# Kernel tuning notes

Hardware: AMD Instinct MI355X
Metric: run time of the kernel (lower is better)

Reference implementation:

```python
import jax, jax.numpy as jnp
import numpy as np

N = 1_000_000   # total nodes
H = 128         # hidden_dim
B = 16_384      # num graphs in batch


def setup_inputs() -> dict:
    key = jax.random.key(0)
    k0, k1, k2, k3 = jax.random.split(key, 4)
    x = jax.random.normal(k0, (N, H), dtype=jnp.float32)
    batch_index = jnp.sort(jax.random.randint(k1, (N,), 0, B))
    s = 1.0 / np.sqrt(H)
    W1 = jax.random.normal(k2, (H, H), dtype=jnp.float32) * s
    b1 = jnp.zeros((H,), dtype=jnp.float32)
    W2 = jax.random.normal(k3, (H, 1), dtype=jnp.float32) * s
    b2 = jnp.zeros((1,), dtype=jnp.float32)
    return {"x": x, "W1": W1, "b1": b1, "W2": W2, "b2": b2,
            "batch_index": batch_index, "num_graphs": B}


def reference(x, W1, b1, W2, b2, batch_index, num_graphs):
    # --- global mean pool ---
    seg_sum = jax.ops.segment_sum(x, batch_index, num_segments=num_graphs)
    counts = jax.ops.segment_sum(jnp.ones((x.shape[0],), x.dtype), batch_index,
                                 num_segments=num_graphs)
    mean = seg_sum / jnp.maximum(counts, 1.0)[:, None]          # [B, H]
    # --- global max pool ---
    mx = jax.ops.segment_max(x, batch_index, num_segments=num_graphs)  # [B, H]
    # --- attentional aggregation: gate MLP -> segment softmax -> weighted sum ---
    h = jax.nn.silu(x @ W1 + b1)                                # [N, H]
    gate = (h @ W2 + b2)[:, 0]                                  # [N]
    gmax = jax.ops.segment_max(gate, batch_index, num_segments=num_graphs)
    e = jnp.exp(gate - gmax[batch_index])
    denom = jax.ops.segment_sum(e, batch_index, num_segments=num_graphs)
    att = e / denom[batch_index]                                # [N] per-segment softmax
    attn_out = jax.ops.segment_sum(att[:, None] * x, batch_index,
                                   num_segments=num_graphs)     # [B, H]
    return jnp.concatenate([mean, mx, attn_out], axis=-1)       # [B, 3H]
```

## Files before the change

### kernel.cpp

```cpp
#include <hip/hip_runtime.h>
#include <hip/hip_bf16.h>
#include <math.h>

#define H 128
#define TILE 64
#define XB_STRIDE 136

typedef __attribute__((ext_vector_type(8))) short bf16x8;
typedef __attribute__((ext_vector_type(4))) float f32x4;

__device__ __forceinline__ short f2bf(float f) {
  union { float f; unsigned u; } v; v.f = f;
  unsigned r = v.u + 0x7fffu + ((v.u >> 16) & 1u);
  return (short)(r >> 16);
}

__global__ void prep_kernel(const float* __restrict__ w1, short* __restrict__ w1t) {
  int i = blockIdx.x * blockDim.x + threadIdx.x;
  if (i >= H * H) return;
  int k = i >> 7, n = i & (H - 1);
  w1t[n * H + k] = f2bf(w1[k * H + n]);
}

__global__ void bounds_kernel(const int* __restrict__ bi, int* __restrict__ seg_start,
                              int N, int B) {
  int n = blockIdx.x * blockDim.x + threadIdx.x;
  if (n >= N) return;
  int cur = bi[n];
  int prev = (n == 0) ? -1 : bi[n - 1];
  for (int g = prev + 1; g <= cur; ++g) seg_start[g] = n;
  if (n == N - 1) {
    for (int g = cur + 1; g <= B; ++g) seg_start[g] = N;
  }
}

__global__ __launch_bounds__(256) void fused_kernel(
    const float* __restrict__ x, const short* __restrict__ w1t,
    const float* __restrict__ b1, const float* __restrict__ w2,
    const float* __restrict__ b2, const int* __restrict__ seg_start,
    float* __restrict__ out)
{
  __shared__ __align__(16) float xf[TILE][H];
  __shared__ __align__(16) short xb[TILE * XB_STRIDE];
  __shared__ float gate_lds[TILE];
  __shared__ float merge_lds[5][H];

  const int g = blockIdx.x;
  const int s = seg_start[g];
  const int e = seg_start[g + 1];
  const int R = e - s;

  const int tid  = threadIdx.x;
  const int w    = tid >> 6;
  const int lane = tid & 63;
  const int l15  = lane & 15;
  const int q    = lane >> 4;

  const int h    = tid & (H - 1);
  const int half = tid >> 7;
  float sum = 0.f, mx = -INFINITY;
  float m_run = -INFINITY, l_run = 0.f, accv = 0.f;

  const float b2v  = b2[0];
  const int   c0   = 32 * w + l15, c1 = c0 + 16;
  const float w2c0 = w2[c0], w2c1 = w2[c1];
  const float b1c0 = b1[c0], b1c1 = b1[c1];

  for (int t0 = 0; t0 < R; t0 += TILE) {
    const int Rt = min(TILE, R - t0);

    {
      const int colg = (tid & 31) * 4;
      const int row0 = tid >> 5;
#pragma unroll
      for (int i = 0; i < 8; ++i) {
        int row = row0 + 8 * i;
        float4 v = make_float4(0.f, 0.f, 0.f, 0.f);
        if (row < Rt) v = *(const float4*)(x + (size_t)(s + t0 + row) * H + colg);
        *(float4*)(&xf[row][colg]) = v;
        short4 sv = make_short4(f2bf(v.x), f2bf(v.y), f2bf(v.z), f2bf(v.w));
        *(short4*)(&xb[row * XB_STRIDE + colg]) = sv;
      }
    }
    if (tid < TILE) gate_lds[tid] = 0.0f;
    __syncthreads();

    f32x4 acc[4][2] = {};
#pragma unroll
    for (int kc = 0; kc < H; kc += 32) {
      bf16x8 a[4], b[2];
#pragma unroll
      for (int mt = 0; mt < 4; ++mt)
        a[mt] = *(const bf16x8*)(&xb[(16 * mt + l15) * XB_STRIDE + kc + 8 * q]);
#pragma unroll
      for (int nt = 0; nt < 2; ++nt) {
        int n = 32 * w + 16 * nt + l15;
        b[nt] = *(const bf16x8*)(w1t + n * H + kc + 8 * q);
      }
#pragma unroll
      for (int mt = 0; mt < 4; ++mt)
#pragma unroll
        for (int nt = 0; nt < 2; ++nt)
          acc[mt][nt] = __builtin_amdgcn_mfma_f32_16x16x32_bf16(a[mt], b[nt], acc[mt][nt], 0, 0, 0);
    }

#pragma unroll
    for (int mt = 0; mt < 4; ++mt) {
#pragma unroll
      for (int r = 0; r < 4; ++r) {
        float h0 = acc[mt][0][r] + b1c0;
        float h1 = acc[mt][1][r] + b1c1;
        float s0 = h0 / (1.0f + __expf(-h0));
        float s1 = h1 / (1.0f + __expf(-h1));
        float p = s0 * w2c0 + s1 * w2c1;
        p += __shfl_xor(p, 1);
        p += __shfl_xor(p, 2);
        p += __shfl_xor(p, 4);
        p += __shfl_xor(p, 8);
        if (l15 == 0) atomicAdd(&gate_lds[16 * mt + 4 * q + r], p);
      }
    }
    __syncthreads();

    for (int r = half; r < Rt; r += 2) {
      float gt = gate_lds[r] + b2v;
      float xv = xf[r][h];
      sum += xv;
      mx = fmaxf(mx, xv);
      float m_new = fmaxf(m_run, gt);
      float corr = __expf(m_run - m_new);
      float ev   = __expf(gt - m_new);
      l_run = l_run * corr + ev;
      accv  = accv * corr + ev * xv;
      m_run = m_new;
    }
    __syncthreads();
  }

  if (half == 1) {
    merge_lds[0][h] = sum;
    merge_lds[1][h] = mx;
    merge_lds[2][h] = m_run;
    merge_lds[3][h] = l_run;
    merge_lds[4][h] = accv;
  }
  __syncthreads();
  if (half == 0) {
    float sum2 = merge_lds[0][h], mx2 = merge_lds[1][h];
    float m2 = merge_lds[2][h], l2 = merge_lds[3][h], a2 = merge_lds[4][h];
    sum += sum2;
    mx = fmaxf(mx, mx2);
    float m_new = fmaxf(m_run, m2);
    float cA = __expf(m_run - m_new);
    float cB = __expf(m2 - m_new);
    l_run = l_run * cA + l2 * cB;
    accv  = accv * cA + a2 * cB;

    float* og = out + (size_t)g * (3 * H);
    og[h]         = sum / fmaxf((float)R, 1.0f);
    og[H + h]     = mx;
    og[2 * H + h] = (R > 0) ? (accv / l_run) : 0.0f;
  }
}

extern "C" void kernel_launch(void* const* d_in, const int* in_sizes, int n_in,
                              void* d_out, int out_size, void* d_ws, size_t ws_size,
                              hipStream_t stream)
{
  const float* x   = (const float*)d_in[0];
  const float* w1  = (const float*)d_in[1];
  const float* b1  = (const float*)d_in[2];
  const float* w2  = (const float*)d_in[3];
  const float* b2  = (const float*)d_in[4];
  const int*  bidx = (const int*)d_in[5];

  const int N  = in_sizes[5];
  const int Bn = out_size / (3 * H);

  char* ws = (char*)d_ws;
  size_t off = 0;
  int* seg_start = (int*)(ws + off);
  off += (size_t)(Bn + 1) * sizeof(int);
  off = (off + 255) & ~(size_t)255;
  short* w1t = (short*)(ws + off);

  prep_kernel<<<(H * H + 255) / 256, 256, 0, stream>>>(w1, w1t);
  bounds_kernel<<<(N + 255) / 256, 256, 0, stream>>>(bidx, seg_start, N, Bn);
  fused_kernel<<<Bn, 256, 0, stream>>>(x, w1t, b1, w2, b2, seg_start, (float*)d_out);
}
```

Before: 884.0 us.

## Keep x tile in registers and compute tile-wide softmax instead of per-row online

Drops the fp32 x tile from LDS. Each thread now keeps its 8 float4 rows in registers and accumulates sum and max as it loads them. The gate reduction changes from shuffles plus LDS atomics to a padded partial-sum buffer reduced by one wave, which also computes a per-tile max and exp weights. The slow per-row serial online softmax is replaced by one rescale per tile, and MFMA work for empty 16-row subtiles is skipped. Occupancy hint 4 is added. The trade is higher register pressure and an extra barrier per tile.

Measured after the change: 1.032 ms. 1.17x slower.

```diff
diff --git a/kernel.cpp b/kernel.cpp
--- a/kernel.cpp
+++ b/kernel.cpp
@@ -5,6 +5,7 @@
 #define H 128
 #define TILE 64
 #define XB_STRIDE 136
+#define PB_STRIDE 68
 
 typedef __attribute__((ext_vector_type(8))) short bf16x8;
 typedef __attribute__((ext_vector_type(4))) float f32x4;
@@ -34,16 +35,16 @@
   }
 }
 
-__global__ __launch_bounds__(256) void fused_kernel(
+__global__ __launch_bounds__(256, 4) void fused_kernel(
     const float* __restrict__ x, const short* __restrict__ w1t,
     const float* __restrict__ b1, const float* __restrict__ w2,
     const float* __restrict__ b2, const int* __restrict__ seg_start,
     float* __restrict__ out)
 {
-  __shared__ __align__(16) float xf[TILE][H];
   __shared__ __align__(16) short xb[TILE * XB_STRIDE];
-  __shared__ float gate_lds[TILE];
-  __shared__ float merge_lds[5][H];
+  __shared__ __align__(16) float pbuf[TILE * PB_STRIDE];
+  __shared__ float w_lds[TILE];
+  __shared__ float bc2[2];
 
   const int g = blockIdx.x;
   const int s = seg_start[g];
@@ -56,10 +57,13 @@
   const int l15  = lane & 15;
   const int q    = lane >> 4;
 
-  const int h    = tid & (H - 1);
-  const int half = tid >> 7;
-  float sum = 0.f, mx = -INFINITY;
-  float m_run = -INFINITY, l_run = 0.f, accv = 0.f;
+  const int c4 = (tid & 31) * 4;
+  const int rb = tid >> 5;
+
+  float4 sum4 = make_float4(0.f, 0.f, 0.f, 0.f);
+  float4 mx4  = make_float4(-INFINITY, -INFINITY, -INFINITY, -INFINITY);
+  float4 av4  = make_float4(0.f, 0.f, 0.f, 0.f);
+  float m_run = -INFINITY, l_run = 0.f;
 
   const float b2v  = b2[0];
   const int   c0   = 32 * w + l15, c1 = c0 + 16;
@@ -67,22 +71,25 @@
   const float b1c0 = b1[c0], b1c1 = b1[c1];
 
   for (int t0 = 0; t0 < R; t0 += TILE) {
-    const int Rt = min(TILE, R - t0);
-
-    {
-      const int colg = (tid & 31) * 4;
-      const int row0 = tid >> 5;
-#pragma unroll
-      for (int i = 0; i < 8; ++i) {
-        int row = row0 + 8 * i;
-        float4 v = make_float4(0.f, 0.f, 0.f, 0.f);
-        if (row < Rt) v = *(const float4*)(x + (size_t)(s + t0 + row) * H + colg);
-        *(float4*)(&xf[row][colg]) = v;
-        short4 sv = make_short4(f2bf(v.x), f2bf(v.y), f2bf(v.z), f2bf(v.w));
-        *(short4*)(&xb[row * XB_STRIDE + colg]) = sv;
-      }
-    }
-    if (tid < TILE) gate_lds[tid] = 0.0f;
+    const int Rt    = min(TILE, R - t0);
+    const int mtMax = (Rt + 15) >> 4;
+
+    float4 xr[8];
+#pragma unroll
+    for (int i = 0; i < 8; ++i) {
+      const int row = rb + 8 * i;
+      const bool valid = row < Rt;
+      float4 v = make_float4(0.f, 0.f, 0.f, 0.f);
+      if (valid) v = *(const float4*)(x + (size_t)(s + t0 + row) * H + c4);
+      xr[i] = v;
+      sum4.x += v.x; sum4.y += v.y; sum4.z += v.z; sum4.w += v.w;
+      if (valid) {
+        mx4.x = fmaxf(mx4.x, v.x); mx4.y = fmaxf(mx4.y, v.y);
+        mx4.z = fmaxf(mx4.z, v.z); mx4.w = fmaxf(mx4.w, v.w);
+      }
+      short4 sv = make_short4(f2bf(v.x), f2bf(v.y), f2bf(v.z), f2bf(v.w));
+      *(short4*)(&xb[row * XB_STRIDE + c4]) = sv;
+    }
     __syncthreads();
 
     f32x4 acc[4][2] = {};
@@ -91,7 +98,8 @@
       bf16x8 a[4], b[2];
 #pragma unroll
       for (int mt = 0; mt < 4; ++mt)
-        a[mt] = *(const bf16x8*)(&xb[(16 * mt + l15) * XB_STRIDE + kc + 8 * q]);
+        if (mt < mtMax)
+          a[mt] = *(const bf16x8*)(&xb[(16 * mt + l15) * XB_STRIDE + kc + 8 * q]);
 #pragma unroll
       for (int nt = 0; nt < 2; ++nt) {
         int n = 32 * w + 16 * nt + l15;
@@ -99,67 +107,85 @@
       }
 #pragma unroll
       for (int mt = 0; mt < 4; ++mt)
-#pragma unroll
-        for (int nt = 0; nt < 2; ++nt)
-          acc[mt][nt] = __builtin_amdgcn_mfma_f32_16x16x32_bf16(a[mt], b[nt], acc[mt][nt], 0, 0, 0);
+        if (mt < mtMax)
+#pragma unroll
+          for (int nt = 0; nt < 2; ++nt)
+            acc[mt][nt] = __builtin_amdgcn_mfma_f32_16x16x32_bf16(a[mt], b[nt], acc[mt][nt], 0, 0, 0);
     }
 
 #pragma unroll
     for (int mt = 0; mt < 4; ++mt) {
-#pragma unroll
-      for (int r = 0; r < 4; ++r) {
-        float h0 = acc[mt][0][r] + b1c0;
-        float h1 = acc[mt][1][r] + b1c1;
-        float s0 = h0 / (1.0f + __expf(-h0));
-        float s1 = h1 / (1.0f + __expf(-h1));
-        float p = s0 * w2c0 + s1 * w2c1;
-        p += __shfl_xor(p, 1);
-        p += __shfl_xor(p, 2);
-        p += __shfl_xor(p, 4);
-        p += __shfl_xor(p, 8);
-        if (l15 == 0) atomicAdd(&gate_lds[16 * mt + 4 * q + r], p);
+      if (mt < mtMax) {
+#pragma unroll
+        for (int r = 0; r < 4; ++r) {
+          float h0 = acc[mt][0][r] + b1c0;
+          float h1 = acc[mt][1][r] + b1c1;
+          float s0 = h0 / (1.0f + __expf(-h0));
+          float s1 = h1 / (1.0f + __expf(-h1));
+          pbuf[(16 * mt + 4 * q + r) * PB_STRIDE + 16 * w + l15] = s0 * w2c0 + s1 * w2c1;
+        }
       }
     }
     __syncthreads();
 
-    for (int r = half; r < Rt; r += 2) {
-      float gt = gate_lds[r] + b2v;
-      float xv = xf[r][h];
-      sum += xv;
-      mx = fmaxf(mx, xv);
-      float m_new = fmaxf(m_run, gt);
-      float corr = __expf(m_run - m_new);
-      float ev   = __expf(gt - m_new);
-      l_run = l_run * corr + ev;
-      accv  = accv * corr + ev * xv;
-      m_run = m_new;
+    if (tid < 64) {
+      const int row = tid;
+      float4 t4 = make_float4(0.f, 0.f, 0.f, 0.f);
+#pragma unroll
+      for (int j = 0; j < 16; ++j) {
+        float4 pv = *(const float4*)(&pbuf[row * PB_STRIDE + 4 * j]);
+        t4.x += pv.x; t4.y += pv.y; t4.z += pv.z; t4.w += pv.w;
+      }
+      const float gate = (t4.x + t4.y) + (t4.z + t4.w) + b2v;
+      const bool valid = row < Rt;
+      float gm = valid ? gate : -INFINITY;
+#pragma unroll
+      for (int m = 1; m < 64; m <<= 1) gm = fmaxf(gm, __shfl_xor(gm, m));
+      const float m_new = fmaxf(m_run, gm);
+      const float wv = valid ? __expf(gate - m_new) : 0.f;
+      w_lds[row] = wv;
+      float tl = wv;
+#pragma unroll
+      for (int m = 1; m < 64; m <<= 1) tl += __shfl_xor(tl, m);
+      if (tid == 0) { bc2[0] = m_new; bc2[1] = tl; }
     }
     __syncthreads();
-  }
-
-  if (half == 1) {
-    merge_lds[0][h] = sum;
-    merge_lds[1][h] = mx;
-    merge_lds[2][h] = m_run;
-    merge_lds[3][h] = l_run;
-    merge_lds[4][h] = accv;
+
+    const float m_new = bc2[0];
+    const float tl    = bc2[1];
+    const float corr  = __expf(m_run - m_new);
+    m_run = m_new;
+    l_run = l_run * corr + tl;
+    av4.x *= corr; av4.y *= corr; av4.z *= corr; av4.w *= corr;
+#pragma unroll
+    for (int i = 0; i < 8; ++i) {
+      const float wv = w_lds[rb + 8 * i];
+      av4.x += wv * xr[i].x; av4.y += wv * xr[i].y;
+      av4.z += wv * xr[i].z; av4.w += wv * xr[i].w;
+    }
+  }
+
+  float* mb = pbuf;
+  {
+    const int base = rb * 136 + c4;
+    *(float4*)(&mb[       base]) = sum4;
+    *(float4*)(&mb[1088 + base]) = mx4;
+    *(float4*)(&mb[2176 + base]) = av4;
   }
   __syncthreads();
-  if (half == 0) {
-    float sum2 = merge_lds[0][h], mx2 = merge_lds[1][h];
-    float m2 = merge_lds[2][h], l2 = merge_lds[3][h], a2 = merge_lds[4][h];
-    sum += sum2;
-    mx = fmaxf(mx, mx2);
-    float m_new = fmaxf(m_run, m2);
-    float cA = __expf(m_run - m_new);
-    float cB = __expf(m2 - m_new);
-    l_run = l_run * cA + l2 * cB;
-    accv  = accv * cA + a2 * cB;
-
+  if (tid < H) {
+    const int c = tid;
+    float sv = 0.f, mv = -INFINITY, av = 0.f;
+#pragma unroll
+    for (int r8 = 0; r8 < 8; ++r8) {
+      sv += mb[r8 * 136 + c];
+      mv  = fmaxf(mv, mb[1088 + r8 * 136 + c]);
+      av += mb[2176 + r8 * 136 + c];
+    }
     float* og = out + (size_t)g * (3 * H);
-    og[h]         = sum / fmaxf((float)R, 1.0f);
-    og[H + h]     = mx;
-    og[2 * H + h] = (R > 0) ? (accv / l_run) : 0.0f;
+    og[c]         = sv / fmaxf((float)R, 1.0f);
+    og[H + c]     = mv;
+    og[2 * H + c] = (R > 0) ? (av / l_run) : 0.0f;
   }
 }
 
```
